# Optimization experiments

Measured on AMD Instinct MI355X. Metric: run time of the kernel, lower is better.

The kernel has to match this reference:

```python
import jax, jax.numpy as jnp
import numpy as np

IN, H, OUT = 28, 64, 10


def _rnn_layer(x_proj, W_hh):
    # x_proj: [T, B, H] time-major, already x @ W_ih^T + b_ih + b_hh
    B = x_proj.shape[1]
    h0 = jnp.zeros((B, H), dtype=x_proj.dtype)

    def step(h, xt):
        h = jnp.tanh(xt + h @ W_hh.T)
        return h, h

    _, hs = jax.lax.scan(step, h0, x_proj)
    return hs  # [T, B, H]


def setup_inputs() -> dict:
    key = jax.random.key(0)
    ks = jax.random.split(key, 12)
    s = 1.0 / np.sqrt(H)  # PyTorch RNN init scale
    B, T = 4096, 256
    return {
        "x": jax.random.normal(ks[0], (B, T, IN), dtype=jnp.float32),
        "W_ih0": jax.random.uniform(ks[1], (H, IN), minval=-s, maxval=s),
        "W_hh0": jax.random.uniform(ks[2], (H, H), minval=-s, maxval=s),
        "b_ih0": jax.random.uniform(ks[3], (H,), minval=-s, maxval=s),
        "b_hh0": jax.random.uniform(ks[4], (H,), minval=-s, maxval=s),
        "W_ih1": jax.random.uniform(ks[5], (H, H), minval=-s, maxval=s),
        "W_hh1": jax.random.uniform(ks[6], (H, H), minval=-s, maxval=s),
        "b_ih1": jax.random.uniform(ks[7], (H,), minval=-s, maxval=s),
        "b_hh1": jax.random.uniform(ks[8], (H,), minval=-s, maxval=s),
        "W_fc": jax.random.uniform(ks[9], (OUT, H), minval=-s, maxval=s),
        "b_fc": jax.random.uniform(ks[10], (OUT,), minval=-s, maxval=s),
    }


def reference(x, W_ih0, W_hh0, b_ih0, b_hh0, W_ih1, W_hh1, b_ih1, b_hh1, W_fc, b_fc):
    # Layer 0: batch input projection as one big GEMM, then sequential scan
    xt = jnp.swapaxes(x, 0, 1)                      # [T, B, IN]
    p0 = xt @ W_ih0.T + (b_ih0 + b_hh0)             # [T, B, H]
    h0_seq = _rnn_layer(p0, W_hh0)                  # [T, B, H]
    # Layer 1
    p1 = h0_seq @ W_ih1.T + (b_ih1 + b_hh1)         # [T, B, H]
    h1_seq = _rnn_layer(p1, W_hh1)                  # [T, B, H]
    # fc on last timestep
    return h1_seq[-1] @ W_fc.T + b_fc               # [B, OUT]
```

## Files before the change

### kernel.cpp

```cpp
#include <hip/hip_runtime.h>

#define TT   256
#define INH  28
#define HH   64
#define OUTN 10

__device__ __forceinline__ float fast_tanh(float x) {
    float cx = fminf(fmaxf(x, -15.0f), 15.0f);
    float e2 = __expf(2.0f * cx);
    return 1.0f - 2.0f * __builtin_amdgcn_rcpf(e2 + 1.0f);
}

__global__ __launch_bounds__(128, 3)
void rnn2_split(const float* __restrict__ x,
                const float* __restrict__ Wih0, const float* __restrict__ Whh0,
                const float* __restrict__ bih0, const float* __restrict__ bhh0,
                const float* __restrict__ Wih1, const float* __restrict__ Whh1,
                const float* __restrict__ bih1, const float* __restrict__ bhh1,
                const float* __restrict__ Wfc,  const float* __restrict__ bfc,
                float* __restrict__ out)
{
    __shared__ __align__(16) float ring[2][2][HH];
    __shared__ __align__(16) float h1s[2][HH];
    __shared__ __align__(16) float xl[2][64];

    const int tid  = threadIdx.x;
    const int lane = tid & 63;
    const int wave = tid >> 6;
    const int b0 = (int)blockIdx.x * 2;
    const int b1 = b0 + 1;

    float wA[HH], wB[HH];
    float bias;
    if (wave == 0) {
#pragma unroll
        for (int k = 0; k < HH; ++k) wA[k] = Whh0[lane * HH + k];
#pragma unroll
        for (int k = 0; k < INH; ++k) wB[k] = Wih0[lane * INH + k];
#pragma unroll
        for (int k = INH; k < HH; ++k) wB[k] = 0.0f;
        bias = bih0[lane] + bhh0[lane];
    } else {
#pragma unroll
        for (int k = 0; k < HH; ++k) wA[k] = Whh1[lane * HH + k];
#pragma unroll
        for (int k = 0; k < HH; ++k) wB[k] = Wih1[lane * HH + k];
        bias = bih1[lane] + bhh1[lane];
    }

    int xrow = (lane < INH) ? b0 : b1;
    int xcol = (lane < INH) ? lane : (lane - INH);
    if (lane >= 2 * INH) { xrow = b1; xcol = INH - 1; }
    const float* xbase = x + (size_t)xrow * (TT * INH) + xcol;

    if (wave == 0) {
        ring[0][0][lane] = 0.0f; ring[0][1][lane] = 0.0f;
        ring[1][0][lane] = 0.0f; ring[1][1][lane] = 0.0f;
        xl[0][lane] = xbase[0];
    } else {
        h1s[0][lane] = 0.0f; h1s[1][lane] = 0.0f;
    }
    __syncthreads();

    float nh00 = 0.0f, nh01 = 0.0f;

    const float4* h1q0 = (const float4*)h1s[0];
    const float4* h1q1 = (const float4*)h1s[1];

#pragma unroll 1
    for (int t = 0; t <= TT + 1; ++t) {
        if (wave == 0) {
            if (t >= 1 && t <= TT) {
                ring[(t - 1) & 1][0][lane] = nh00;
                ring[(t - 1) & 1][1][lane] = nh01;
            }
            if (t < TT) {
                const int tn = (t + 1 < TT) ? (t + 1) : (TT - 1);
                const float xv = xbase[(size_t)tn * INH];
                const float4* xq = (const float4*)xl[t & 1];
                const float4* s0 = (const float4*)ring[(t + 1) & 1][0];
                const float4* s1 = (const float4*)ring[(t + 1) & 1][1];
                float pa0 = bias, pb0 = 0.0f, pa1 = bias, pb1 = 0.0f;
#pragma unroll
                for (int i = 0; i < 7; ++i) {
                    float4 a = xq[i], b = xq[7 + i];
                    pa0 = fmaf(a.x, wB[4*i+0], pa0); pa1 = fmaf(b.x, wB[4*i+0], pa1);
                    pb0 = fmaf(a.y, wB[4*i+1], pb0); pb1 = fmaf(b.y, wB[4*i+1], pb1);
                    pa0 = fmaf(a.z, wB[4*i+2], pa0); pa1 = fmaf(b.z, wB[4*i+2], pa1);
                    pb0 = fmaf(a.w, wB[4*i+3], pb0); pb1 = fmaf(b.w, wB[4*i+3], pb1);
                }
#pragma unroll
                for (int kk = 0; kk < 16; ++kk) {
                    float4 a = s0[kk], b = s1[kk];
                    pa0 = fmaf(a.x, wA[4*kk+0], pa0); pa1 = fmaf(b.x, wA[4*kk+0], pa1);
                    pb0 = fmaf(a.y, wA[4*kk+1], pb0); pb1 = fmaf(b.y, wA[4*kk+1], pb1);
                    pa0 = fmaf(a.z, wA[4*kk+2], pa0); pa1 = fmaf(b.z, wA[4*kk+2], pa1);
                    pb0 = fmaf(a.w, wA[4*kk+3], pb0); pb1 = fmaf(b.w, wA[4*kk+3], pb1);
                }
                nh00 = fast_tanh(pa0 + pb0);
                nh01 = fast_tanh(pa1 + pb1);
                xl[(t + 1) & 1][lane] = xv;
            }
        } else {
            if (t >= 2) {
                const float4* s0 = (const float4*)ring[t & 1][0];
                const float4* s1 = (const float4*)ring[t & 1][1];
                float qa0 = bias, qb0 = 0.0f, qa1 = bias, qb1 = 0.0f;
#pragma unroll
                for (int kk = 0; kk < 16; ++kk) {
                    float4 a = s0[kk], b = s1[kk];
                    qa0 = fmaf(a.x, wB[4*kk+0], qa0); qa1 = fmaf(b.x, wB[4*kk+0], qa1);
                    qb0 = fmaf(a.y, wB[4*kk+1], qb0); qb1 = fmaf(b.y, wB[4*kk+1], qb1);
                    qa0 = fmaf(a.z, wB[4*kk+2], qa0); qa1 = fmaf(b.z, wB[4*kk+2], qa1);
                    qb0 = fmaf(a.w, wB[4*kk+3], qb0); qb1 = fmaf(b.w, wB[4*kk+3], qb1);
                }
#pragma unroll
                for (int kk = 0; kk < 16; ++kk) {
                    float4 c = h1q0[kk], d = h1q1[kk];
                    qa0 = fmaf(c.x, wA[4*kk+0], qa0); qa1 = fmaf(d.x, wA[4*kk+0], qa1);
                    qb0 = fmaf(c.y, wA[4*kk+1], qb0); qb1 = fmaf(d.y, wA[4*kk+1], qb1);
                    qa0 = fmaf(c.z, wA[4*kk+2], qa0); qa1 = fmaf(d.z, wA[4*kk+2], qa1);
                    qb0 = fmaf(c.w, wA[4*kk+3], qb0); qb1 = fmaf(d.w, wA[4*kk+3], qb1);
                }
                h1s[0][lane] = fast_tanh(qa0 + qb0);
                h1s[1][lane] = fast_tanh(qa1 + qb1);
            }
        }
        __syncthreads();
    }

    if (wave == 1 && lane < OUTN) {
        const float4* wrow = (const float4*)(Wfc + lane * HH);
        float acc0 = bfc[lane];
        float acc1 = acc0;
#pragma unroll
        for (int kk = 0; kk < 16; ++kk) {
            float4 w = wrow[kk];
            float4 a = h1q0[kk], b = h1q1[kk];
            acc0 = fmaf(a.x, w.x, acc0); acc1 = fmaf(b.x, w.x, acc1);
            acc0 = fmaf(a.y, w.y, acc0); acc1 = fmaf(b.y, w.y, acc1);
            acc0 = fmaf(a.z, w.z, acc0); acc1 = fmaf(b.z, w.z, acc1);
            acc0 = fmaf(a.w, w.w, acc0); acc1 = fmaf(b.w, w.w, acc1);
        }
        out[(size_t)b0 * OUTN + lane] = acc0;
        out[(size_t)b1 * OUTN + lane] = acc1;
    }
}

extern "C" void kernel_launch(void* const* d_in, const int* in_sizes, int n_in,
                              void* d_out, int out_size, void* d_ws, size_t ws_size,
                              hipStream_t stream) {
    const float* x    = (const float*)d_in[0];
    const float* Wih0 = (const float*)d_in[1];
    const float* Whh0 = (const float*)d_in[2];
    const float* bih0 = (const float*)d_in[3];
    const float* bhh0 = (const float*)d_in[4];
    const float* Wih1 = (const float*)d_in[5];
    const float* Whh1 = (const float*)d_in[6];
    const float* bih1 = (const float*)d_in[7];
    const float* bhh1 = (const float*)d_in[8];
    const float* Wfc  = (const float*)d_in[9];
    const float* bfc  = (const float*)d_in[10];
    float* out = (float*)d_out;

    rnn2_split<<<2048, 128, 0, stream>>>(x, Wih0, Whh0, bih0, bhh0,
                                         Wih1, Whh1, bih1, bhh1, Wfc, bfc, out);
}
```

Baseline: 692.1 us.

## Split RNN into four-stage wave pipeline processing four batch rows per block

Restructures the kernel so each block handles four batch rows with four waves, each wave owning one matrix (input projection, layer-0 recurrence, layer-1 input projection, layer-1 recurrence) in a software pipeline through double-buffered shared memory. Each wave holds only one 64-wide weight row in registers instead of two, which lowers register pressure and lets more waves reside per SIMU. Wave roles are rotated by block index to spread the work across SIMDs. In exchange, the pipeline is one stage deeper and every wave must pass through a block barrier each step.

```diff
diff --git a/kernel.cpp b/kernel.cpp
--- a/kernel.cpp
+++ b/kernel.cpp
@@ -4,6 +4,7 @@
 #define INH  28
 #define HH   64
 #define OUTN 10
+#define ROWS 4
 
 __device__ __forceinline__ float fast_tanh(float x) {
     float cx = fminf(fmaxf(x, -15.0f), 15.0f);
@@ -11,8 +12,9 @@
     return 1.0f - 2.0f * __builtin_amdgcn_rcpf(e2 + 1.0f);
 }
 
-__global__ __launch_bounds__(128, 3)
-void rnn2_split(const float* __restrict__ x,
+__global__ __launch_bounds__(256)
+__attribute__((amdgpu_waves_per_eu(4, 4)))
+void rnn2_pipe4(const float* __restrict__ x,
                 const float* __restrict__ Wih0, const float* __restrict__ Whh0,
                 const float* __restrict__ bih0, const float* __restrict__ bhh0,
                 const float* __restrict__ Wih1, const float* __restrict__ Whh1,
@@ -20,130 +22,166 @@
                 const float* __restrict__ Wfc,  const float* __restrict__ bfc,
                 float* __restrict__ out)
 {
-    __shared__ __align__(16) float ring[2][2][HH];
-    __shared__ __align__(16) float h1s[2][HH];
-    __shared__ __align__(16) float xl[2][64];
+    __shared__ __align__(16) float xl [2][ROWS][32];
+    __shared__ __align__(16) float xpR[2][ROWS][HH];
+    __shared__ __align__(16) float h0R[2][ROWS][HH];
+    __shared__ __align__(16) float uR [2][ROWS][HH];
+    __shared__ __align__(16) float h1R[2][ROWS][HH];
 
     const int tid  = threadIdx.x;
     const int lane = tid & 63;
-    const int wave = tid >> 6;
-    const int b0 = (int)blockIdx.x * 2;
-    const int b1 = b0 + 1;
-
-    float wA[HH], wB[HH];
-    float bias;
-    if (wave == 0) {
-#pragma unroll
-        for (int k = 0; k < HH; ++k) wA[k] = Whh0[lane * HH + k];
-#pragma unroll
-        for (int k = 0; k < INH; ++k) wB[k] = Wih0[lane * INH + k];
-#pragma unroll
-        for (int k = INH; k < HH; ++k) wB[k] = 0.0f;
-        bias = bih0[lane] + bhh0[lane];
+    const int wv   = tid >> 6;
+    const int role = (wv + (int)blockIdx.x) & 3;
+    const int b0   = (int)blockIdx.x * ROWS;
+
+    float w[HH];
+    if (role == 0) {
+#pragma unroll
+        for (int k = 0; k < INH; ++k) w[k] = Wih0[lane * INH + k];
+#pragma unroll
+        for (int k = INH; k < HH; ++k) w[k] = 0.0f;
     } else {
-#pragma unroll
-        for (int k = 0; k < HH; ++k) wA[k] = Whh1[lane * HH + k];
-#pragma unroll
-        for (int k = 0; k < HH; ++k) wB[k] = Wih1[lane * HH + k];
-        bias = bih1[lane] + bhh1[lane];
-    }
-
-    int xrow = (lane < INH) ? b0 : b1;
-    int xcol = (lane < INH) ? lane : (lane - INH);
-    if (lane >= 2 * INH) { xrow = b1; xcol = INH - 1; }
-    const float* xbase = x + (size_t)xrow * (TT * INH) + xcol;
-
-    if (wave == 0) {
-        ring[0][0][lane] = 0.0f; ring[0][1][lane] = 0.0f;
-        ring[1][0][lane] = 0.0f; ring[1][1][lane] = 0.0f;
-        xl[0][lane] = xbase[0];
-    } else {
-        h1s[0][lane] = 0.0f; h1s[1][lane] = 0.0f;
+        const float* wsrc = (role == 1) ? Whh0 : (role == 2) ? Wih1 : Whh1;
+#pragma unroll
+        for (int k = 0; k < HH; ++k) w[k] = wsrc[lane * HH + k];
+    }
+    float bias = 0.0f;
+    if (role == 0) bias = bih0[lane] + bhh0[lane];
+    if (role == 3) bias = bih1[lane] + bhh1[lane];
+
+    const int row0 = lane / INH, col0 = lane - row0 * INH;
+    const int e1 = lane + 64;
+    const int row1g = e1 / INH, col1 = e1 - row1g * INH;
+    const int row1 = (row1g < ROWS) ? row1g : (ROWS - 1);
+    const float* px0 = x + (size_t)(b0 + row0) * (TT * INH) + col0;
+    const float* px1 = x + (size_t)(b0 + row1) * (TT * INH) + col1;
+
+    for (int i = tid; i < 2 * ROWS * HH; i += 256) {
+        ((float*)h0R)[i] = 0.0f;
+        ((float*)h1R)[i] = 0.0f;
+    }
+    if (role == 0) {
+        xl[0][row0][col0] = px0[0];
+        if (lane < 48) xl[0][row1][col1] = px1[0];
     }
     __syncthreads();
 
-    float nh00 = 0.0f, nh01 = 0.0f;
-
-    const float4* h1q0 = (const float4*)h1s[0];
-    const float4* h1q1 = (const float4*)h1s[1];
-
 #pragma unroll 1
-    for (int t = 0; t <= TT + 1; ++t) {
-        if (wave == 0) {
-            if (t >= 1 && t <= TT) {
-                ring[(t - 1) & 1][0][lane] = nh00;
-                ring[(t - 1) & 1][1][lane] = nh01;
-            }
+    for (int t = 0; t <= TT + 2; ++t) {
+        if (role == 0) {
             if (t < TT) {
                 const int tn = (t + 1 < TT) ? (t + 1) : (TT - 1);
-                const float xv = xbase[(size_t)tn * INH];
-                const float4* xq = (const float4*)xl[t & 1];
-                const float4* s0 = (const float4*)ring[(t + 1) & 1][0];
-                const float4* s1 = (const float4*)ring[(t + 1) & 1][1];
-                float pa0 = bias, pb0 = 0.0f, pa1 = bias, pb1 = 0.0f;
-#pragma unroll
-                for (int i = 0; i < 7; ++i) {
-                    float4 a = xq[i], b = xq[7 + i];
-                    pa0 = fmaf(a.x, wB[4*i+0], pa0); pa1 = fmaf(b.x, wB[4*i+0], pa1);
-                    pb0 = fmaf(a.y, wB[4*i+1], pb0); pb1 = fmaf(b.y, wB[4*i+1], pb1);
-                    pa0 = fmaf(a.z, wB[4*i+2], pa0); pa1 = fmaf(b.z, wB[4*i+2], pa1);
-                    pb0 = fmaf(a.w, wB[4*i+3], pb0); pb1 = fmaf(b.w, wB[4*i+3], pb1);
-                }
-#pragma unroll
-                for (int kk = 0; kk < 16; ++kk) {
-                    float4 a = s0[kk], b = s1[kk];
-                    pa0 = fmaf(a.x, wA[4*kk+0], pa0); pa1 = fmaf(b.x, wA[4*kk+0], pa1);
-                    pb0 = fmaf(a.y, wA[4*kk+1], pb0); pb1 = fmaf(b.y, wA[4*kk+1], pb1);
-                    pa0 = fmaf(a.z, wA[4*kk+2], pa0); pa1 = fmaf(b.z, wA[4*kk+2], pa1);
-                    pb0 = fmaf(a.w, wA[4*kk+3], pb0); pb1 = fmaf(b.w, wA[4*kk+3], pb1);
-                }
-                nh00 = fast_tanh(pa0 + pb0);
-                nh01 = fast_tanh(pa1 + pb1);
-                xl[(t + 1) & 1][lane] = xv;
+                const float xv0 = px0[(size_t)tn * INH];
+                float xv1 = 0.0f;
+                if (lane < 48) xv1 = px1[(size_t)tn * INH];
+
+                float xpv[ROWS];
+#pragma unroll
+                for (int r = 0; r < ROWS; ++r) {
+                    const float4* xq = (const float4*)xl[t & 1][r];
+                    float a0 = bias, a1 = 0.0f;
+#pragma unroll
+                    for (int i = 0; i < 7; ++i) {
+                        float4 v = xq[i];
+                        a0 = fmaf(v.x, w[4*i+0], a0);
+                        a1 = fmaf(v.y, w[4*i+1], a1);
+                        a0 = fmaf(v.z, w[4*i+2], a0);
+                        a1 = fmaf(v.w, w[4*i+3], a1);
+                    }
+                    xpv[r] = a0 + a1;
+                }
+#pragma unroll
+                for (int r = 0; r < ROWS; ++r) xpR[t & 1][r][lane] = xpv[r];
+                xl[(t + 1) & 1][row0][col0] = xv0;
+                if (lane < 48) xl[(t + 1) & 1][row1][col1] = xv1;
+            }
+        } else if (role == 1) {
+            if (t >= 1 && t <= TT) {
+                const int sw = (t - 1) & 1;
+                const int sr = t & 1;
+                float hv[ROWS];
+#pragma unroll
+                for (int r = 0; r < ROWS; ++r) {
+                    float a0 = xpR[sw][r][lane], a1 = 0.0f;
+                    const float4* hq = (const float4*)h0R[sr][r];
+#pragma unroll
+                    for (int kk = 0; kk < 16; ++kk) {
+                        float4 v = hq[kk];
+                        a0 = fmaf(v.x, w[4*kk+0], a0);
+                        a1 = fmaf(v.y, w[4*kk+1], a1);
+                        a0 = fmaf(v.z, w[4*kk+2], a0);
+                        a1 = fmaf(v.w, w[4*kk+3], a1);
+                    }
+                    hv[r] = fast_tanh(a0 + a1);
+                }
+#pragma unroll
+                for (int r = 0; r < ROWS; ++r) h0R[sw][r][lane] = hv[r];
+            }
+        } else if (role == 2) {
+            if (t >= 2 && t <= TT + 1) {
+                const int sr = t & 1;
+                float uv[ROWS];
+#pragma unroll
+                for (int r = 0; r < ROWS; ++r) {
+                    float a0 = 0.0f, a1 = 0.0f;
+                    const float4* hq = (const float4*)h0R[sr][r];
+#pragma unroll
+                    for (int kk = 0; kk < 16; ++kk) {
+                        float4 v = hq[kk];
+                        a0 = fmaf(v.x, w[4*kk+0], a0);
+                        a1 = fmaf(v.y, w[4*kk+1], a1);
+                        a0 = fmaf(v.z, w[4*kk+2], a0);
+                        a1 = fmaf(v.w, w[4*kk+3], a1);
+                    }
+                    uv[r] = a0 + a1;
+                }
+#pragma unroll
+                for (int r = 0; r < ROWS; ++r) uR[sr][r][lane] = uv[r];
             }
         } else {
-            if (t >= 2) {
-                const float4* s0 = (const float4*)ring[t & 1][0];
-                const float4* s1 = (const float4*)ring[t & 1][1];
-                float qa0 = bias, qb0 = 0.0f, qa1 = bias, qb1 = 0.0f;
-#pragma unroll
-                for (int kk = 0; kk < 16; ++kk) {
-                    float4 a = s0[kk], b = s1[kk];
-                    qa0 = fmaf(a.x, wB[4*kk+0], qa0); qa1 = fmaf(b.x, wB[4*kk+0], qa1);
-                    qb0 = fmaf(a.y, wB[4*kk+1], qb0); qb1 = fmaf(b.y, wB[4*kk+1], qb1);
-                    qa0 = fmaf(a.z, wB[4*kk+2], qa0); qa1 = fmaf(b.z, wB[4*kk+2], qa1);
-                    qb0 = fmaf(a.w, wB[4*kk+3], qb0); qb1 = fmaf(b.w, wB[4*kk+3], qb1);
-                }
-#pragma unroll
-                for (int kk = 0; kk < 16; ++kk) {
-                    float4 c = h1q0[kk], d = h1q1[kk];
-                    qa0 = fmaf(c.x, wA[4*kk+0], qa0); qa1 = fmaf(d.x, wA[4*kk+0], qa1);
-                    qb0 = fmaf(c.y, wA[4*kk+1], qb0); qb1 = fmaf(d.y, wA[4*kk+1], qb1);
-                    qa0 = fmaf(c.z, wA[4*kk+2], qa0); qa1 = fmaf(d.z, wA[4*kk+2], qa1);
-                    qb0 = fmaf(c.w, wA[4*kk+3], qb0); qb1 = fmaf(d.w, wA[4*kk+3], qb1);
-                }
-                h1s[0][lane] = fast_tanh(qa0 + qb0);
-                h1s[1][lane] = fast_tanh(qa1 + qb1);
+            if (t >= 3) {
+                const int su = (t - 1) & 1;
+                const int sr = t & 1;
+                float hv[ROWS];
+#pragma unroll
+                for (int r = 0; r < ROWS; ++r) {
+                    float a0 = uR[su][r][lane] + bias, a1 = 0.0f;
+                    const float4* hq = (const float4*)h1R[sr][r];
+#pragma unroll
+                    for (int kk = 0; kk < 16; ++kk) {
+                        float4 v = hq[kk];
+                        a0 = fmaf(v.x, w[4*kk+0], a0);
+                        a1 = fmaf(v.y, w[4*kk+1], a1);
+                        a0 = fmaf(v.z, w[4*kk+2], a0);
+                        a1 = fmaf(v.w, w[4*kk+3], a1);
+                    }
+                    hv[r] = fast_tanh(a0 + a1);
+                }
+#pragma unroll
+                for (int r = 0; r < ROWS; ++r) h1R[su][r][lane] = hv[r];
             }
         }
         __syncthreads();
     }
 
-    if (wave == 1 && lane < OUTN) {
+    if (role == 3 && lane < OUTN) {
         const float4* wrow = (const float4*)(Wfc + lane * HH);
-        float acc0 = bfc[lane];
-        float acc1 = acc0;
-#pragma unroll
-        for (int kk = 0; kk < 16; ++kk) {
-            float4 w = wrow[kk];
-            float4 a = h1q0[kk], b = h1q1[kk];
-            acc0 = fmaf(a.x, w.x, acc0); acc1 = fmaf(b.x, w.x, acc1);
-            acc0 = fmaf(a.y, w.y, acc0); acc1 = fmaf(b.y, w.y, acc1);
-            acc0 = fmaf(a.z, w.z, acc0); acc1 = fmaf(b.z, w.z, acc1);
-            acc0 = fmaf(a.w, w.w, acc0); acc1 = fmaf(b.w, w.w, acc1);
+        const float bf = bfc[lane];
+#pragma unroll
+        for (int r = 0; r < ROWS; ++r) {
+            const float4* hq = (const float4*)h1R[(TT - 1) & 1][r];
+            float a0 = bf, a1 = 0.0f;
+#pragma unroll
+            for (int kk = 0; kk < 16; ++kk) {
+                float4 wv = wrow[kk];
+                float4 hvv = hq[kk];
+                a0 = fmaf(hvv.x, wv.x, a0);
+                a1 = fmaf(hvv.y, wv.y, a1);
+                a0 = fmaf(hvv.z, wv.z, a0);
+                a1 = fmaf(hvv.w, wv.w, a1);
+            }
+            out[(size_t)(b0 + r) * OUTN + lane] = a0 + a1;
         }
-        out[(size_t)b0 * OUTN + lane] = acc0;
-        out[(size_t)b1 * OUTN + lane] = acc1;
     }
 }
 
@@ -163,6 +201,6 @@
     const float* bfc  = (const float*)d_in[10];
     float* out = (float*)d_out;
 
-    rnn2_split<<<2048, 128, 0, stream>>>(x, Wih0, Whh0, bih0, bhh0,
+    rnn2_pipe4<<<1024, 256, 0, stream>>>(x, Wih0, Whh0, bih0, bhh0,
                                          Wih1, Whh1, bih1, bhh1, Wfc, bfc, out);
 }
```

New measurement: 641.3 us. -7.3%, faster.
